# Optimization experiments

Measured on AMD Instinct MI355X. Metric: run time of the kernel, lower is better.

Reference implementation:

```python
import jax, jax.numpy as jnp
import numpy as np

NUM_HEADS = 8
ATTN_BALANCE = 0.5
EPS = 1e-4  # eps in normalize()


def mp_linear(x, w, gain):
    # MP_Conv with kernel=(1,1): per-output-channel RMS weight renorm then scale.
    # normalize(w): w / (eps + ||w_row|| / sqrt(fan_in)); then * gain / sqrt(fan_in)
    fan_in = w.shape[1]
    n = jnp.linalg.norm(w.astype(jnp.float32), axis=1, keepdims=True)  # (out,1)
    wn = w / (EPS + n / np.sqrt(fan_in))
    wn = wn * (gain / np.sqrt(fan_in))
    return x @ wn.T


def setup_inputs() -> dict:
    key = jax.random.key(0)
    ks = jax.random.split(key, 6)
    B, S, E = 8, 1024, 1024
    H = NUM_HEADS
    return {
        "query": jax.random.normal(ks[0], (B, S, E), jnp.float32),
        "gain_s": jnp.ones((), jnp.float32),
        "gain_t": jnp.ones((), jnp.float32),
        "q_w": jax.random.normal(ks[1], (E, E), jnp.float32),
        "k_w": jax.random.normal(ks[2], (E, E), jnp.float32),
        "v_w": jax.random.normal(ks[3], (E, E), jnp.float32),
        "o_w": jax.random.normal(ks[4], (E, E), jnp.float32),
        "rel_pos_bias": 0.01 * jax.random.normal(ks[5], (H, S, S), jnp.float32),
    }


def reference(query, gain_s, gain_t, q_w, k_w, v_w, o_w, rel_pos_bias):
    # time_dim=0 so the time-dependent branches are inactive; gain_t unused.
    B, S, E = query.shape
    H = NUM_HEADS
    hd = E // H
    # MP projections (1x1 conv == per-position linear), split heads -> (B,H,S,hd)
    q = mp_linear(query, q_w, gain_s).reshape(B, S, H, hd).transpose(0, 2, 1, 3)
    k = mp_linear(query, k_w, gain_s).reshape(B, S, H, hd).transpose(0, 2, 1, 3)
    v = mp_linear(query, v_w, gain_s).reshape(B, S, H, hd).transpose(0, 2, 1, 3)
    # (B,H,S,S) scores, scaled, plus learned relative position bias (seq_len == seq_ln)
    scores = jnp.einsum("bhsd,bhtd->bhst", q, k) / np.sqrt(hd) + rel_pos_bias[None]
    attn = jax.nn.softmax(scores, axis=-1)
    o = jnp.einsum("bhst,bhtd->bhsd", attn, v)
    o = o.transpose(0, 2, 1, 3).reshape(B, S, E)
    out = mp_linear(o, o_w, gain_s)
    # mp_sum residual: lerp(res, out, t) / sqrt((1-t)^2 + t^2)
    t = ATTN_BALANCE
    return (query * (1.0 - t) + out * t) / np.sqrt((1.0 - t) ** 2 + t ** 2)
```

## Files before the change

kernel.cpp:

```cpp
#include <hip/hip_runtime.h>
#include <hip/hip_bf16.h>
#include <math.h>


typedef __attribute__((ext_vector_type(4))) float f32x4;
typedef __attribute__((ext_vector_type(4))) short s16x4;
typedef __attribute__((ext_vector_type(8))) short s16x8;

__device__ __forceinline__ short f2bf(float f) {
  union { __hip_bfloat16 h; short s; } u;
  u.h = __float2bfloat16(f);
  return u.s;
}
__device__ __forceinline__ float bf2f(short s) {
  union { short s; __hip_bfloat16 h; } u;
  u.s = s;
  return __bfloat162float(u.h);
}
__device__ __forceinline__ f32x4 mfma16(s16x8 a, s16x8 b, f32x4 c) {
  return __builtin_amdgcn_mfma_f32_16x16x32_bf16(a, b, c, 0, 0, 0);
}

typedef __attribute__((address_space(1))) const unsigned int* as1_u32p;
typedef __attribute__((address_space(3))) unsigned int* as3_u32p;
__device__ __forceinline__ void g2l16(const short* g, short* l) {
  __builtin_amdgcn_global_load_lds((as1_u32p)g, (as3_u32p)l, 16, 0, 0);
}

#define ASM_VMCNT0 asm volatile("s_waitcnt vmcnt(0)" ::: "memory")
#define ASM_LGKM0  asm volatile("s_waitcnt lgkmcnt(0)" ::: "memory")
#define SFENCE     __builtin_amdgcn_sched_barrier(0)
#define BARRIER    __builtin_amdgcn_s_barrier()

__global__ __launch_bounds__(256) void k_wnorm(const float* __restrict__ qw, const float* __restrict__ kw,
                                               const float* __restrict__ vw, const float* __restrict__ ow,
                                               const float* __restrict__ gain, short* __restrict__ wn) {
  const int r = blockIdx.x;
  const int mat = r >> 10;
  const float* W = mat == 0 ? qw : mat == 1 ? kw : mat == 2 ? vw : ow;
  const float* src = W + (size_t)(r & 1023) * 1024;
  const int tid = threadIdx.x;
  f32x4 v = *(const f32x4*)&src[tid * 4];
  float s = v[0]*v[0] + v[1]*v[1] + v[2]*v[2] + v[3]*v[3];
  __shared__ float red[256];
  red[tid] = s; __syncthreads();
  for (int off = 128; off > 0; off >>= 1) {
    if (tid < off) red[tid] += red[tid + off];
    __syncthreads();
  }
  const float scale = gain[0] / (0.0032f + sqrtf(red[0]));
  s16x4 o;
  o[0] = f2bf(v[0]*scale); o[1] = f2bf(v[1]*scale);
  o[2] = f2bf(v[2]*scale); o[3] = f2bf(v[3]*scale);
  *(s16x4*)&wn[(size_t)r * 1024 + tid * 4] = o;
}

__global__ __launch_bounds__(256) void k_cvt(const float* __restrict__ in, short* __restrict__ out, int n4) {
  int idx = blockIdx.x * 256 + threadIdx.x;
  int stride = gridDim.x * 256;
  for (int i = idx; i < n4; i += stride) {
    f32x4 v = ((const f32x4*)in)[i];
    s16x4 o;
    o[0] = f2bf(v[0]); o[1] = f2bf(v[1]); o[2] = f2bf(v[2]); o[3] = f2bf(v[3]);
    ((s16x4*)out)[i] = o;
  }
}

__global__ __launch_bounds__(256) void k_scaleb(const float* __restrict__ in, short* __restrict__ out, int n4) {
  const float L2E = 1.4426950408889634f;
  int idx = blockIdx.x * 256 + threadIdx.x;
  int stride = gridDim.x * 256;
  for (int i = idx; i < n4; i += stride) {
    f32x4 v = ((const f32x4*)in)[i];
    s16x4 o;
    o[0] = f2bf(v[0]*L2E); o[1] = f2bf(v[1]*L2E);
    o[2] = f2bf(v[2]*L2E); o[3] = f2bf(v[3]*L2E);
    ((s16x4*)out)[i] = o;
  }
}

#define GEMM_K_LOOP(XPTR, WPTR)                                                      \
  const int srw = lane >> 3;                                  \
  const int ssl = lane & 7;                                            \
  const int ql7 = ql & 7;                                                            \
  {                                                                                  \
    _Pragma("unroll")                                                                \
    for (int i = 0; i < 4; i++) {                                                    \
      const int row = i * 32 + w * 8 + srw;                                          \
      g2l16(&XPTR[(size_t)(m0 + row) * 1024 + ((ssl ^ srw) << 3)],                   \
            &Al[0][(i * 32 + w * 8) * 64]);                                          \
      g2l16(&WPTR[(size_t)(n0 + row) * 1024 + ((ssl ^ srw) << 3)],                   \
            &Bl[0][(i * 32 + w * 8) * 64]);                                          \
    }                                                                                \
    ASM_VMCNT0; SFENCE; BARRIER; SFENCE;                                             \
    int bi = 0;                                                                      \
    for (int t = 0; t < 16; ++t) {                                                   \
      if (t < 15) {                                                                  \
        const int k1 = (t + 1) * 64;                                                 \
        _Pragma("unroll")                                                            \
        for (int i = 0; i < 4; i++) {                                                \
          const int row = i * 32 + w * 8 + srw;                                      \
          g2l16(&XPTR[(size_t)(m0 + row) * 1024 + k1 + ((ssl ^ srw) << 3)],          \
                &Al[bi ^ 1][(i * 32 + w * 8) * 64]);                                 \
          g2l16(&WPTR[(size_t)(n0 + row) * 1024 + k1 + ((ssl ^ srw) << 3)],          \
                &Bl[bi ^ 1][(i * 32 + w * 8) * 64]);                                 \
        }                                                                            \
      }                                                                              \
      const char* alp = (const char*)&Al[bi][0];                                     \
      const char* blp = (const char*)&Bl[bi][0];                                     \
      __builtin_amdgcn_s_setprio(1);                                                 \
      _Pragma("unroll")                                                              \
      for (int kc = 0; kc < 2; ++kc) {                                               \
        s16x8 af[4], bfr[4];                                                         \
        _Pragma("unroll")                                                            \
        for (int i = 0; i < 4; i++) {                                                \
          const int rA = wm * 64 + i * 16 + ql;                                      \
          af[i] = *(const s16x8*)(alp + rA * 128 +                                   \
                                  ((kc * 64 + 16 * hi) ^ (ql7 << 4)));               \
        }                                                                            \
        _Pragma("unroll")                                                            \
        for (int j = 0; j < 4; j++) {                                                \
          const int rB = wn_ * 64 + j * 16 + ql;                                     \
          bfr[j] = *(const s16x8*)(blp + rB * 128 +                                  \
                                   ((kc * 64 + 16 * hi) ^ (ql7 << 4)));              \
        }                                                                            \
        _Pragma("unroll")                                                            \
        for (int i = 0; i < 4; i++)                                                  \
          _Pragma("unroll")                                                          \
          for (int j = 0; j < 4; j++) acc[i][j] = mfma16(af[i], bfr[j], acc[i][j]);  \
      }                                                                              \
      __builtin_amdgcn_s_setprio(0);                                                 \
      ASM_VMCNT0; SFENCE; BARRIER; SFENCE;                                           \
      bi ^= 1;                                                                       \
    }                                                                                \
  }

__global__ __launch_bounds__(256) void k_gemm_qkv(const short* __restrict__ X, const short* __restrict__ WN,
                                                  short* __restrict__ Qb, short* __restrict__ Kb,
                                                  short* __restrict__ Vt) {
  __shared__ short Al[2][128 * 64];
  __shared__ short Bl[2][128 * 64];
  const int z = blockIdx.z;
  const short* __restrict__ Wm = WN + (size_t)z * 1048576;
  const int m0 = blockIdx.x * 128, n0 = blockIdx.y * 128;
  const int tid = threadIdx.x, lane = tid & 63, w = tid >> 6;
  const int hi = lane >> 4, ql = lane & 15;
  const int wm = w >> 1, wn_ = w & 1;
  f32x4 acc[4][4];
#pragma unroll
  for (int i = 0; i < 4; i++)
#pragma unroll
    for (int j = 0; j < 4; j++) acc[i][j] = (f32x4){0.f, 0.f, 0.f, 0.f};
  GEMM_K_LOOP(X, Wm)
  short* Cl = &Al[0][0];
  if (z == 2) {
#pragma unroll
    for (int i = 0; i < 4; i++) {
#pragma unroll
      for (int j = 0; j < 4; j++) {
        int col = wn_ * 64 + j * 16 + ql;
        int rowb = wm * 64 + i * 16 + 4 * hi;
#pragma unroll
        for (int r = 0; r < 4; r++) Cl[col * 128 + rowb + r] = f2bf(acc[i][j][r]);
      }
    }
    __syncthreads();
    const int b = m0 >> 10, sb = (m0 & 1023);
#pragma unroll
    for (int it = 0; it < 8; ++it) {
      int idx = tid + it * 256;
      int dl = idx >> 4, c = idx & 15;
      int ng = n0 + dl, h = ng >> 7, d = ng & 127;
      *(s16x8*)&Vt[(size_t)((b * 8 + h) * 128 + d) * 1024 + sb + c * 8] =
          *(const s16x8*)&Cl[dl * 128 + c * 8];
    }
  } else {
    short* __restrict__ C = (z == 0) ? Qb : Kb;
#pragma unroll
    for (int i = 0; i < 4; i++) {
#pragma unroll
      for (int j = 0; j < 4; j++) {
        int col = wn_ * 64 + j * 16 + ql;
        int rowb = wm * 64 + i * 16 + 4 * hi;
#pragma unroll
        for (int r = 0; r < 4; r++) Cl[(rowb + r) * 128 + col] = f2bf(acc[i][j][r]);
      }
    }
    __syncthreads();
#pragma unroll
    for (int it = 0; it < 8; ++it) {
      int idx = tid + it * 256;
      int row = idx >> 4, c = idx & 15;
      *(s16x8*)&C[(size_t)(m0 + row) * 1024 + n0 + c * 8] = *(const s16x8*)&Cl[row * 128 + c * 8];
    }
  }
}

__global__ __launch_bounds__(256) void k_attn(const short* __restrict__ Qb, const short* __restrict__ Kb,
                                              const short* __restrict__ Vt, const short* __restrict__ B2,
                                              short* __restrict__ Ob) {
  __shared__ short lds[64 * 128 + 128 * 64];
  short* Kl = lds;
  short* Vl = lds + 64 * 128;
  int f = blockIdx.x + (blockIdx.y << 4);
  f = (f & 7) * 128 + (f >> 3);
  const int bh = f >> 4, b = bh >> 3, h = bh & 7;
  const int q0 = (f & 15) * 64;
  const int tid = threadIdx.x, w = tid >> 6, lane = tid & 63;
  const int hi = lane >> 4, ql = lane & 15, ql7 = ql & 7;
  const int qrow = q0 + w * 16 + ql;
  const short* __restrict__ qbase = Qb + (size_t)(b * 1024 + qrow) * 1024 + h * 128;
  s16x8 qf[4];
#pragma unroll
  for (int kc = 0; kc < 4; kc++) qf[kc] = *(const s16x8*)&qbase[kc * 32 + 8 * hi];
  float lsum = 0.f;
  f32x4 acc[8];
#pragma unroll
  for (int d = 0; d < 8; d++) acc[d] = (f32x4){0.f, 0.f, 0.f, 0.f};
  const float sc2 = (float)(0.08838834764831845 * 1.4426950408889634);
  const int krow_ = tid >> 4, kslot = tid & 15;
  const int vrow_ = tid >> 3, vslot = tid & 7;
  const short* __restrict__ Kg = Kb + (size_t)(b * 1024) * 1024 + h * 128;
  const short* __restrict__ Vg = Vt + (size_t)bh * 128 * 1024;
  const short* __restrict__ Bg = B2 + (size_t)(h * 1024 + qrow) * 1024;

  s16x8 krA[4], vrA[4], krB[4], vrB[4];
  s16x4 brA[4], brB[4];
#define LOADT(KR, VR, BR, T0)                                                          \
  do {                                                                                 \
    _Pragma("unroll")                                                                  \
    for (int i = 0; i < 4; i++)                                                        \
      KR[i] = *(const s16x8*)&Kg[(size_t)((T0) + i * 16 + krow_) * 1024 + kslot * 8];  \
    _Pragma("unroll")                                                                  \
    for (int i = 0; i < 4; i++)                                                        \
      VR[i] = *(const s16x8*)&Vg[(size_t)(i * 32 + vrow_) * 1024 + (T0) + vslot * 8];  \
    _Pragma("unroll")                                                                  \
    for (int t = 0; t < 4; t++)                                                        \
      BR[t] = *(const s16x4*)&Bg[(T0) + t * 16 + 4 * hi];                              \
  } while (0)

#define STAGE(KR, VR)                                                                  \
  do {                                                                                 \
    _Pragma("unroll")                                                                  \
    for (int i = 0; i < 4; i++) {                                                      \
      int row = i * 16 + krow_;                                                        \
      *(s16x8*)((char*)Kl + row * 256 + ((kslot ^ (row & 7)) << 4)) = KR[i];           \
    }                                                                                  \
    _Pragma("unroll")                                                                  \
    for (int i = 0; i < 4; i++) {                                                      \
      int row = i * 32 + vrow_;                                                        \
      *(s16x8*)((char*)Vl + row * 128 + ((vslot ^ (row & 7)) << 4)) = VR[i];           \
    }                                                                                  \
  } while (0)

#define COMPUTE(BR)                                                                    \
  do {                                                                                 \
    f32x4 st[4];                                                                       \
    __builtin_amdgcn_s_setprio(1);                                                     \
    _Pragma("unroll")                                                                  \
    for (int tb = 0; tb < 4; tb++) {                                                   \
      st[tb] = (f32x4){0.f, 0.f, 0.f, 0.f};                                            \
      _Pragma("unroll")                                                                \
      for (int kc = 0; kc < 4; kc++) {                                                 \
        s16x8 kf = *(const s16x8*)((const char*)Kl + (tb * 16 + ql) * 256 +            \
                                   ((kc * 64 + 16 * hi) ^ (ql7 << 4)));                \
        st[tb] = mfma16(kf, qf[kc], st[tb]);                                           \
      }                                                                                \
    }                                                                                  \
    __builtin_amdgcn_s_setprio(0);                                                     \
    s16x8 pf[2];                                                                       \
    _Pragma("unroll")                                                                  \
    for (int tc = 0; tc < 2; tc++) {                                                   \
      _Pragma("unroll")                                                                \
      for (int r = 0; r < 4; r++) {                                                    \
        float e0 = exp2f(fmaf(st[2 * tc][r],     sc2, bf2f(BR[2 * tc][r])));           \
        float e1 = exp2f(fmaf(st[2 * tc + 1][r], sc2, bf2f(BR[2 * tc + 1][r])));       \
        lsum += e0 + e1;                                                               \
        pf[tc][r] = f2bf(e0);                                                          \
        pf[tc][4 + r] = f2bf(e1);                                                      \
      }                                                                                \
    }                                                                                  \
    __builtin_amdgcn_s_setprio(1);                                                     \
    _Pragma("unroll")                                                                  \
    for (int db = 0; db < 8; db++) {                                                   \
      const char* vbase = (const char*)Vl + (db * 16 + ql) * 128;                      \
      _Pragma("unroll")                                                                \
      for (int tc = 0; tc < 2; tc++) {                                                 \
        s16x4 lo  = *(const s16x4*)(vbase + ((tc * 64 + 8 * hi) ^ (ql7 << 4)));        \
        s16x4 hi4 = *(const s16x4*)(vbase + ((tc * 64 + 32 + 8 * hi) ^ (ql7 << 4)));   \
        s16x8 vf;                                                                      \
        vf[0] = lo[0]; vf[1] = lo[1]; vf[2] = lo[2]; vf[3] = lo[3];                    \
        vf[4] = hi4[0]; vf[5] = hi4[1]; vf[6] = hi4[2]; vf[7] = hi4[3];                 \
        acc[db] = mfma16(vf, pf[tc], acc[db]);                                         \
      }                                                                                \
    }                                                                                  \
    __builtin_amdgcn_s_setprio(0);                                                     \
  } while (0)

  LOADT(krA, vrA, brA, 0);
  for (int ih = 0; ih < 8; ++ih) {
    const int t0 = ih * 128;
    ASM_VMCNT0; SFENCE;
    STAGE(krA, vrA);
    LOADT(krB, vrB, brB, t0 + 64);
    ASM_LGKM0; SFENCE; BARRIER; SFENCE;
    COMPUTE(brA);
    BARRIER; SFENCE;
    ASM_VMCNT0; SFENCE;
    STAGE(krB, vrB);
    if (ih < 7) LOADT(krA, vrA, brA, t0 + 128);
    ASM_LGKM0; SFENCE; BARRIER; SFENCE;
    COMPUTE(brB);
    BARRIER; SFENCE;
  }
  lsum += __shfl_xor(lsum, 16);
  lsum += __shfl_xor(lsum, 32);
  const float invl = 1.f / lsum;
  short* Ol = lds;
#pragma unroll
  for (int db = 0; db < 8; db++) {
    s16x4 v;
    v[0] = f2bf(acc[db][0] * invl); v[1] = f2bf(acc[db][1] * invl);
    v[2] = f2bf(acc[db][2] * invl); v[3] = f2bf(acc[db][3] * invl);
    *(s16x4*)&Ol[(w * 16 + ql) * 136 + db * 16 + 4 * hi] = v;
  }
  __syncthreads();
#pragma unroll
  for (int it = 0; it < 4; ++it) {
    int idx = tid + it * 256;
    int row = idx >> 4, c = idx & 15;
    *(s16x8*)&Ob[(size_t)(b * 1024 + q0 + row) * 1024 + h * 128 + c * 8] = *(const s16x8*)&Ol[row * 136 + c * 8];
  }
#undef LOADT
#undef STAGE
#undef COMPUTE
}

__global__ __launch_bounds__(256) void k_gemm_o(const short* __restrict__ X, const short* __restrict__ Wm,
                                                const float* __restrict__ Qin, float* __restrict__ Out) {
  __shared__ short Al[2][128 * 64];
  __shared__ short Bl[2][128 * 64];
  const int m0 = blockIdx.x * 128, n0 = blockIdx.y * 128;
  const int tid = threadIdx.x, lane = tid & 63, w = tid >> 6;
  const int hi = lane >> 4, ql = lane & 15;
  const int wm = w >> 1, wn_ = w & 1;
  f32x4 acc[4][4];
#pragma unroll
  for (int i = 0; i < 4; i++)
#pragma unroll
    for (int j = 0; j < 4; j++) acc[i][j] = (f32x4){0.f, 0.f, 0.f, 0.f};
  GEMM_K_LOOP(X, Wm)
#pragma unroll
  for (int i = 0; i < 4; i++) {
    int mg = m0 + wm * 64 + i * 16 + 4 * hi;
#pragma unroll
    for (int j = 0; j < 4; j++) {
      int ng = n0 + wn_ * 64 + j * 16 + ql;
#pragma unroll
      for (int r = 0; r < 4; r++) {
        size_t idx = (size_t)(mg + r) * 1024 + ng;
        Out[idx] = (Qin[idx] + acc[i][j][r]) * 0.7071067811865476f;
      }
    }
  }
}

extern "C" void kernel_launch(void* const* d_in, const int* in_sizes, int n_in,
                              void* d_out, int out_size, void* d_ws, size_t ws_size,
                              hipStream_t stream) {
  (void)in_sizes; (void)n_in; (void)out_size; (void)ws_size;
  const float* query = (const float*)d_in[0];
  const float* gain_s = (const float*)d_in[1];
  const float* qw = (const float*)d_in[3];
  const float* kw = (const float*)d_in[4];
  const float* vw = (const float*)d_in[5];
  const float* ow = (const float*)d_in[6];
  const float* bias = (const float*)d_in[7];
  float* out = (float*)d_out;

  short* ws = (short*)d_ws;
  short* s_wn = ws;
  short* s_x  = s_wn + 4 * 1048576;
  short* s_B2 = s_x + 8388608;
  short* s_Q  = s_B2 + 8388608;
  short* s_K  = s_Q + 8388608;
  short* s_Vt = s_K + 8388608;
  short* s_O  = s_x;

  k_wnorm<<<dim3(4096), dim3(256), 0, stream>>>(qw, kw, vw, ow, gain_s, s_wn);
  k_cvt<<<dim3(2048), dim3(256), 0, stream>>>(query, s_x, 2097152);
  k_scaleb<<<dim3(2048), dim3(256), 0, stream>>>(bias, s_B2, 2097152);
  k_gemm_qkv<<<dim3(64, 8, 3), dim3(256), 0, stream>>>(s_x, s_wn, s_Q, s_K, s_Vt);
  k_attn<<<dim3(16, 64), dim3(256), 0, stream>>>(s_Q, s_K, s_Vt, s_B2, s_O);
  k_gemm_o<<<dim3(64, 8), dim3(256), 0, stream>>>(s_O, s_wn + 3 * 1048576, query, out);
}
```

Measured before the change: 307.9 us.

## Switch attention kernel to 32x32x16 MFMA with 128-query tiles

Rewrites the attention kernel to use 32x32x16 bf16 MFMA instead of 16x16x32, with each wave handling 32 query rows so a block covers 128 queries and the grid halves. Each staged K/V tile is reused by twice as many queries, halving K/V global and LDS traffic per query. The V staging layout, bias loads (moved into compute), P fragment packing and output swizzle are reworked to match the new fragment layout. This raises register pressure (larger accumulators and Q fragments), which may lower occupancy, and the smaller grid of 512 blocks may leave some CUs underused.

```diff
diff --git a/kernel.cpp b/kernel.cpp
--- a/kernel.cpp
+++ b/kernel.cpp
@@ -4,6 +4,7 @@
 
 
 typedef __attribute__((ext_vector_type(4))) float f32x4;
+typedef __attribute__((ext_vector_type(16))) float f32x16;
 typedef __attribute__((ext_vector_type(4))) short s16x4;
 typedef __attribute__((ext_vector_type(8))) short s16x8;
 
@@ -19,6 +20,9 @@
 }
 __device__ __forceinline__ f32x4 mfma16(s16x8 a, s16x8 b, f32x4 c) {
   return __builtin_amdgcn_mfma_f32_16x16x32_bf16(a, b, c, 0, 0, 0);
+}
+__device__ __forceinline__ f32x16 mfma32(s16x8 a, s16x8 b, f32x16 c) {
+  return __builtin_amdgcn_mfma_f32_32x32x16_bf16(a, b, c, 0, 0, 0);
 }
 
 typedef __attribute__((address_space(1))) const unsigned int* as1_u32p;
@@ -202,31 +206,33 @@
   __shared__ short lds[64 * 128 + 128 * 64];
   short* Kl = lds;
   short* Vl = lds + 64 * 128;
-  int f = blockIdx.x + (blockIdx.y << 4);
-  f = (f & 7) * 128 + (f >> 3);
-  const int bh = f >> 4, b = bh >> 3, h = bh & 7;
-  const int q0 = (f & 15) * 64;
+  int f = blockIdx.x + (blockIdx.y << 3);
+  f = (f & 7) * 64 + (f >> 3);
+  const int bh = f >> 3, b = bh >> 3, h = bh & 7;
+  const int q0 = (f & 7) * 128;
   const int tid = threadIdx.x, w = tid >> 6, lane = tid & 63;
-  const int hi = lane >> 4, ql = lane & 15, ql7 = ql & 7;
-  const int qrow = q0 + w * 16 + ql;
+  const int l31 = lane & 31, hi2 = lane >> 5, sw = l31 & 7;
+  const int qrow = q0 + w * 32 + l31;
   const short* __restrict__ qbase = Qb + (size_t)(b * 1024 + qrow) * 1024 + h * 128;
-  s16x8 qf[4];
-#pragma unroll
-  for (int kc = 0; kc < 4; kc++) qf[kc] = *(const s16x8*)&qbase[kc * 32 + 8 * hi];
+  s16x8 qf[8];
+#pragma unroll
+  for (int kc = 0; kc < 8; kc++) qf[kc] = *(const s16x8*)&qbase[kc * 16 + hi2 * 8];
   float lsum = 0.f;
-  f32x4 acc[8];
-#pragma unroll
-  for (int d = 0; d < 8; d++) acc[d] = (f32x4){0.f, 0.f, 0.f, 0.f};
+  f32x16 acc[4];
+#pragma unroll
+  for (int db = 0; db < 4; db++)
+#pragma unroll
+    for (int r = 0; r < 16; r++) acc[db][r] = 0.f;
   const float sc2 = (float)(0.08838834764831845 * 1.4426950408889634);
   const int krow_ = tid >> 4, kslot = tid & 15;
   const int vrow_ = tid >> 3, vslot = tid & 7;
+  const int vks = vslot >> 1, vm = vslot & 1;
   const short* __restrict__ Kg = Kb + (size_t)(b * 1024) * 1024 + h * 128;
   const short* __restrict__ Vg = Vt + (size_t)bh * 128 * 1024;
   const short* __restrict__ Bg = B2 + (size_t)(h * 1024 + qrow) * 1024;
 
   s16x8 krA[4], vrA[4], krB[4], vrB[4];
-  s16x4 brA[4], brB[4];
-#define LOADT(KR, VR, BR, T0)                                                          \
+#define LOADT(KR, VR, T0)                                                              \
   do {                                                                                 \
     _Pragma("unroll")                                                                  \
     for (int i = 0; i < 4; i++)                                                        \
@@ -234,9 +240,6 @@
     _Pragma("unroll")                                                                  \
     for (int i = 0; i < 4; i++)                                                        \
       VR[i] = *(const s16x8*)&Vg[(size_t)(i * 32 + vrow_) * 1024 + (T0) + vslot * 8];  \
-    _Pragma("unroll")                                                                  \
-    for (int t = 0; t < 4; t++)                                                        \
-      BR[t] = *(const s16x4*)&Bg[(T0) + t * 16 + 4 * hi];                              \
   } while (0)
 
 #define STAGE(KR, VR)                                                                  \
@@ -249,87 +252,104 @@
     _Pragma("unroll")                                                                  \
     for (int i = 0; i < 4; i++) {                                                      \
       int row = i * 32 + vrow_;                                                        \
-      *(s16x8*)((char*)Vl + row * 128 + ((vslot ^ (row & 7)) << 4)) = VR[i];           \
+      char* vb = (char*)Vl + row * 128;                                                \
+      s16x4 lo, hi4;                                                                   \
+      lo[0] = VR[i][0]; lo[1] = VR[i][1]; lo[2] = VR[i][2]; lo[3] = VR[i][3];          \
+      hi4[0] = VR[i][4]; hi4[1] = VR[i][5]; hi4[2] = VR[i][6]; hi4[3] = VR[i][7];      \
+      *(s16x4*)(vb + (((vks * 2) ^ (row & 7)) << 4) + vm * 8) = lo;                    \
+      *(s16x4*)(vb + (((vks * 2 + 1) ^ (row & 7)) << 4) + vm * 8) = hi4;               \
     }                                                                                  \
   } while (0)
 
-#define COMPUTE(BR)                                                                    \
+#define COMPUTE(T0)                                                                    \
   do {                                                                                 \
-    f32x4 st[4];                                                                       \
+    s16x4 br[8];                           \
+    _Pragma("unroll")                                                                  \
+    for (int tb = 0; tb < 2; tb++)                                                     \
+      _Pragma("unroll")                                                                \
+      for (int u = 0; u < 4; u++)                                                      \
+        br[tb * 4 + u] = *(const s16x4*)&Bg[(T0) + tb * 32 + u * 8 + 4 * hi2];         \
+    f32x16 st[2];                                                                      \
     __builtin_amdgcn_s_setprio(1);                                                     \
     _Pragma("unroll")                                                                  \
-    for (int tb = 0; tb < 4; tb++) {                                                   \
-      st[tb] = (f32x4){0.f, 0.f, 0.f, 0.f};                                            \
-      _Pragma("unroll")                                                                \
-      for (int kc = 0; kc < 4; kc++) {                                                 \
-        s16x8 kf = *(const s16x8*)((const char*)Kl + (tb * 16 + ql) * 256 +            \
-                                   ((kc * 64 + 16 * hi) ^ (ql7 << 4)));                \
-        st[tb] = mfma16(kf, qf[kc], st[tb]);                                           \
+    for (int tb = 0; tb < 2; tb++) {                                                   \
+      _Pragma("unroll")                                                                \
+      for (int r = 0; r < 16; r++) st[tb][r] = 0.f;                                    \
+      _Pragma("unroll")                                                                \
+      for (int kc = 0; kc < 8; kc++) {                                                 \
+        s16x8 kf = *(const s16x8*)((const char*)Kl + (tb * 32 + l31) * 256 +           \
+                                   (((kc * 2 + hi2) ^ sw) << 4));                      \
+        st[tb] = mfma32(kf, qf[kc], st[tb]);                                           \
       }                                                                                \
     }                                                                                  \
     __builtin_amdgcn_s_setprio(0);                                                     \
-    s16x8 pf[2];                                                                       \
-    _Pragma("unroll")                                                                  \
-    for (int tc = 0; tc < 2; tc++) {                                                   \
-      _Pragma("unroll")                                                                \
-      for (int r = 0; r < 4; r++) {                                                    \
-        float e0 = exp2f(fmaf(st[2 * tc][r],     sc2, bf2f(BR[2 * tc][r])));           \
-        float e1 = exp2f(fmaf(st[2 * tc + 1][r], sc2, bf2f(BR[2 * tc + 1][r])));       \
-        lsum += e0 + e1;                                                               \
-        pf[tc][r] = f2bf(e0);                                                          \
-        pf[tc][4 + r] = f2bf(e1);                                                      \
+    _Pragma("unroll")                                                                  \
+    for (int tb = 0; tb < 2; tb++)                                                     \
+      _Pragma("unroll")                                                                \
+      for (int r = 0; r < 16; r++) {                                                   \
+        float e = exp2f(fmaf(st[tb][r], sc2, bf2f(br[tb * 4 + (r >> 2)][r & 3])));     \
+        st[tb][r] = e;                                                                 \
+        lsum += e;                                                                     \
       }                                                                                \
-    }                                                                                  \
+    s16x8 pf[4];                  \
+    _Pragma("unroll")                                                                  \
+    for (int ks = 0; ks < 4; ks++)                                                     \
+      _Pragma("unroll")                                                                \
+      for (int e = 0; e < 8; e++)                                                      \
+        pf[ks][e] = f2bf(st[ks >> 1][(e & 3) + 8 * (ks & 1) + 4 * (e >> 2)]);          \
     __builtin_amdgcn_s_setprio(1);                                                     \
     _Pragma("unroll")                                                                  \
-    for (int db = 0; db < 8; db++) {                                                   \
-      const char* vbase = (const char*)Vl + (db * 16 + ql) * 128;                      \
-      _Pragma("unroll")                                                                \
-      for (int tc = 0; tc < 2; tc++) {                                                 \
-        s16x4 lo  = *(const s16x4*)(vbase + ((tc * 64 + 8 * hi) ^ (ql7 << 4)));        \
-        s16x4 hi4 = *(const s16x4*)(vbase + ((tc * 64 + 32 + 8 * hi) ^ (ql7 << 4)));   \
-        s16x8 vf;                                                                      \
-        vf[0] = lo[0]; vf[1] = lo[1]; vf[2] = lo[2]; vf[3] = lo[3];                    \
-        vf[4] = hi4[0]; vf[5] = hi4[1]; vf[6] = hi4[2]; vf[7] = hi4[3];                 \
-        acc[db] = mfma16(vf, pf[tc], acc[db]);                                         \
+    for (int db = 0; db < 4; db++)                                                     \
+      _Pragma("unroll")                                                                \
+      for (int ks = 0; ks < 4; ks++) {                                                 \
+        s16x8 vf = *(const s16x8*)((const char*)Vl + (db * 32 + l31) * 128 +           \
+                                   (((ks * 2 + hi2) ^ sw) << 4));                      \
+        acc[db] = mfma32(vf, pf[ks], acc[db]);                                         \
       }                                                                                \
-    }                                                                                  \
     __builtin_amdgcn_s_setprio(0);                                                     \
   } while (0)
 
-  LOADT(krA, vrA, brA, 0);
+  LOADT(krA, vrA, 0);
   for (int ih = 0; ih < 8; ++ih) {
     const int t0 = ih * 128;
     ASM_VMCNT0; SFENCE;
     STAGE(krA, vrA);
-    LOADT(krB, vrB, brB, t0 + 64);
+    LOADT(krB, vrB, t0 + 64);
     ASM_LGKM0; SFENCE; BARRIER; SFENCE;
-    COMPUTE(brA);
+    COMPUTE(t0);
     BARRIER; SFENCE;
     ASM_VMCNT0; SFENCE;
     STAGE(krB, vrB);
-    if (ih < 7) LOADT(krA, vrA, brA, t0 + 128);
+    if (ih < 7) LOADT(krA, vrA, t0 + 128);
     ASM_LGKM0; SFENCE; BARRIER; SFENCE;
-    COMPUTE(brB);
+    COMPUTE(t0 + 64);
     BARRIER; SFENCE;
   }
-  lsum += __shfl_xor(lsum, 16);
   lsum += __shfl_xor(lsum, 32);
   const float invl = 1.f / lsum;
+  __syncthreads();
   short* Ol = lds;
-#pragma unroll
-  for (int db = 0; db < 8; db++) {
-    s16x4 v;
-    v[0] = f2bf(acc[db][0] * invl); v[1] = f2bf(acc[db][1] * invl);
-    v[2] = f2bf(acc[db][2] * invl); v[3] = f2bf(acc[db][3] * invl);
-    *(s16x4*)&Ol[(w * 16 + ql) * 136 + db * 16 + 4 * hi] = v;
+  const int qloc = w * 32 + l31, qs = qloc & 7;
+#pragma unroll
+  for (int db = 0; db < 4; db++) {
+#pragma unroll
+    for (int u = 0; u < 4; u++) {
+      int d0 = db * 32 + u * 8 + 4 * hi2;
+      s16x4 v;
+      v[0] = f2bf(acc[db][4 * u + 0] * invl);
+      v[1] = f2bf(acc[db][4 * u + 1] * invl);
+      v[2] = f2bf(acc[db][4 * u + 2] * invl);
+      v[3] = f2bf(acc[db][4 * u + 3] * invl);
+      *(s16x4*)((char*)Ol + qloc * 256 + (((d0 >> 3) ^ qs) << 4) + (d0 & 7) * 2) = v;
+    }
   }
   __syncthreads();
 #pragma unroll
-  for (int it = 0; it < 4; ++it) {
+  for (int it = 0; it < 8; ++it) {
     int idx = tid + it * 256;
     int row = idx >> 4, c = idx & 15;
-    *(s16x8*)&Ob[(size_t)(b * 1024 + q0 + row) * 1024 + h * 128 + c * 8] = *(const s16x8*)&Ol[row * 136 + c * 8];
+    s16x8 vv = *(const s16x8*)((const char*)Ol + row * 256 + ((c ^ (row & 7)) << 4));
+    *(s16x8*)&Ob[(size_t)(b * 1024 + q0 + row) * 1024 + h * 128 + c * 8] = vv;
   }
 #undef LOADT
 #undef STAGE
@@ -391,6 +411,6 @@
   k_cvt<<<dim3(2048), dim3(256), 0, stream>>>(query, s_x, 2097152);
   k_scaleb<<<dim3(2048), dim3(256), 0, stream>>>(bias, s_B2, 2097152);
   k_gemm_qkv<<<dim3(64, 8, 3), dim3(256), 0, stream>>>(s_x, s_wn, s_Q, s_K, s_Vt);
-  k_attn<<<dim3(16, 64), dim3(256), 0, stream>>>(s_Q, s_K, s_Vt, s_B2, s_O);
+  k_attn<<<dim3(8, 64), dim3(256), 0, stream>>>(s_Q, s_K, s_Vt, s_B2, s_O);
   k_gemm_o<<<dim3(64, 8), dim3(256), 0, stream>>>(s_O, s_wn + 3 * 1048576, query, out);
 }
```

Measured after the change: 311.4 us. No clear change (+1.1%).
